# Performance work log

Hardware: AMD Instinct MI355X
Metric: run time of the kernel (lower is better)

The kernel has to match this reference:

```python
import jax, jax.numpy as jnp
import numpy as np

B = 4096      # batch
D = 256       # flattened input feature dim
NUMFEAT = 1 + D + D * (D + 1) // 2  # 33153: bias + linear + quadratic terms


def setup_inputs() -> dict:
    key = jax.random.key(0)
    k1, k2 = jax.random.split(key)
    x = jax.random.normal(k1, (B, D), dtype=jnp.float32)
    # nn.Linear(numfeat, 10, bias=False): weight shape (10, numfeat)
    W = jax.random.normal(k2, (10, NUMFEAT), dtype=jnp.float32) * 0.01
    return {"x": x, "W": W}


def reference(x, W):
    # x: (B, D) -- original does x.view(B, -1); already 2D here.
    b, d = x.shape
    # sklearn PolynomialFeatures(degree=2) column order:
    # [1, x_0..x_{d-1}, x_0*x_0, x_0*x_1, ..., x_{d-1}*x_{d-1}]
    # i.e. combinations_with_replacement == upper-triangular (incl. diagonal)
    iu0, iu1 = np.triu_indices(d)  # static index constants
    ones = jnp.ones((b, 1), dtype=x.dtype)
    cross = x[:, iu0] * x[:, iu1]          # (B, D*(D+1)/2)
    feats = jnp.concatenate([ones, x, cross], axis=1)  # (B, NUMFEAT)
    return feats @ W.T                      # (B, 10)
```

## Files before the change

### kernel.cpp

```cpp
#include <hip/hip_runtime.h>


#define DD 256
#define NF 33153
#define TPB 256
#define ASTRIDE 264

typedef __attribute__((ext_vector_type(8))) short short8;
typedef __attribute__((ext_vector_type(4))) float floatx4;
typedef __attribute__((ext_vector_type(4), aligned(4))) float float4a;

union S8U { unsigned u[4]; short8 s; };

__device__ inline unsigned pack2(float lo, float hi) {
    unsigned a = __builtin_bit_cast(unsigned, hi) + 0x8000u;
    unsigned b = __builtin_bit_cast(unsigned, lo) + 0x8000u;
    return __builtin_amdgcn_perm(a, b, 0x07060302u);
}

__global__ __launch_bounds__(TPB)
void PolynomialRegression_75385265979710_kernel(const float* __restrict__ x,
                                                const float* __restrict__ W,
                                                float* __restrict__ out) {
    __shared__ __align__(16) unsigned short As[64 * ASTRIDE];
    __shared__ float red[4 * 64];

    const int tid  = threadIdx.x;
    const int lane = tid & 63, wave = tid >> 6;
    const int ln   = lane & 15, quad = lane >> 4;
    const int q8   = quad * 8;
    const int rowbase = blockIdx.x * 64;
    const int o  = blockIdx.y;
    const int g1 = wave, g2 = 7 - wave;

#pragma unroll
    for (int it = 0; it < 8; ++it) {
        int idx = it * 2048 + tid * 8;
        int r = idx >> 8, c = idx & 255;
        const float* src = &x[(rowbase + r) * DD + c];
        float4a v0 = *(const float4a*)src;
        float4a v1 = *(const float4a*)(src + 4);
        S8U p;
        p.u[0] = pack2(v0.x, v0.y); p.u[1] = pack2(v0.z, v0.w);
        p.u[2] = pack2(v1.x, v1.y); p.u[3] = pack2(v1.z, v1.w);
        *(short8*)&As[r * ASTRIDE + c] = p.s;
    }
    __syncthreads();

    int iRow[4], bBase[4];
#pragma unroll
    for (int nt = 0; nt < 4; ++nt) {
        int g = (nt < 2) ? g1 : g2;
        int i = g * 32 + (nt & 1) * 16 + ln;
        iRow[nt]  = i;
        bBase[nt] = o * NF + 257 + i * 255 - ((i * (i - 1)) >> 1);
    }

    floatx4 acc[4][4];
#pragma unroll
    for (int mt = 0; mt < 4; ++mt)
#pragma unroll
        for (int nt = 0; nt < 4; ++nt) acc[mt][nt] = (floatx4)0.f;

    auto loadA = [&](int kk, short8* a) {
#pragma unroll
        for (int mt = 0; mt < 4; ++mt)
            a[mt] = *(const short8*)&As[(mt * 16 + ln) * ASTRIDE + kk + q8];
    };
    auto loadB = [&](int nt, int kk) -> short8 {
        const float* p = &W[bBase[nt] + kk + q8];
        float4a w0 = *(const float4a*)p;
        float4a w1 = *(const float4a*)(p + 4);
        S8U r;
        r.u[0] = pack2(w0.x, w0.y); r.u[1] = pack2(w0.z, w0.w);
        r.u[2] = pack2(w1.x, w1.y); r.u[3] = pack2(w1.z, w1.w);
        return r.s;
    };
    auto loadBmask = [&](int nt, int kk) -> short8 {
        int di = iRow[nt] - kk;
        const float* p = &W[bBase[nt] + kk + q8];
        float4a w0 = *(const float4a*)p;
        float4a w1 = *(const float4a*)(p + 4);
        float f[8] = {w0.x, w0.y, w0.z, w0.w, w1.x, w1.y, w1.z, w1.w};
#pragma unroll
        for (int e = 0; e < 8; ++e)
            if (q8 + e < di) f[e] = 0.f;
        S8U r;
        r.u[0] = pack2(f[0], f[1]); r.u[1] = pack2(f[2], f[3]);
        r.u[2] = pack2(f[4], f[5]); r.u[3] = pack2(f[6], f[7]);
        return r.s;
    };
    auto mfma2 = [&](short8* a, short8 b0, short8 b1, int nlo) {
#pragma unroll
        for (int mt = 0; mt < 4; ++mt) {
            acc[mt][nlo]     = __builtin_amdgcn_mfma_f32_16x16x32_bf16(a[mt], b0, acc[mt][nlo],     0, 0, 0);
            acc[mt][nlo + 1] = __builtin_amdgcn_mfma_f32_16x16x32_bf16(a[mt], b1, acc[mt][nlo + 1], 0, 0, 0);
        }
    };

    {
        short8 a[4];
        loadA(g1 * 32, a);
        mfma2(a, loadBmask(0, g1 * 32), loadBmask(1, g1 * 32), 0);
        loadA(g2 * 32, a);
        mfma2(a, loadBmask(2, g2 * 32), loadBmask(3, g2 * 32), 2);
    }
    for (int c = g1 + 1; c <= g2; ++c) {
        short8 a[4];
        loadA(c * 32, a);
        mfma2(a, loadB(0, c * 32), loadB(1, c * 32), 0);
    }
    for (int c = g2 + 1; c < 8; ++c) {
        short8 a[4];
        loadA(c * 32, a);
        mfma2(a, loadB(0, c * 32), loadB(1, c * 32), 0);
        mfma2(a, loadB(2, c * 32), loadB(3, c * 32), 2);
    }

    float w1v[4];
#pragma unroll
    for (int nt = 0; nt < 4; ++nt)
        w1v[nt] = W[o * NF + 1 + iRow[nt]];

#pragma unroll
    for (int mt = 0; mt < 4; ++mt) {
#pragma unroll
        for (int r = 0; r < 4; ++r) {
            const int m = mt * 16 + quad * 4 + r;
            float p = 0.f;
#pragma unroll
            for (int nt = 0; nt < 4; ++nt) {
                float xv = x[(rowbase + m) * DD + iRow[nt]];
                p = fmaf(xv, acc[mt][nt][r] + w1v[nt], p);
            }
            p += __shfl_xor(p, 1);
            p += __shfl_xor(p, 2);
            p += __shfl_xor(p, 4);
            p += __shfl_xor(p, 8);
            if (ln == 0) red[wave * 64 + m] = p;
        }
    }
    __syncthreads();

    if (tid < 64) {
        float s = red[tid] + red[64 + tid] + red[128 + tid] + red[192 + tid] + W[o * NF];
        out[(rowbase + tid) * 10 + o] = s;
    }
}

extern "C" void kernel_launch(void* const* d_in, const int* in_sizes, int n_in,
                              void* d_out, int out_size, void* d_ws, size_t ws_size,
                              hipStream_t stream) {
    const float* x = (const float*)d_in[0];
    const float* W = (const float*)d_in[1];
    float* out = (float*)d_out;

    dim3 grid(4096 / 64, 10);
    PolynomialRegression_75385265979710_kernel<<<grid, TPB, 0, stream>>>(x, W, out);
}
```

Baseline: 71.65 us.

## Prebuild masked bf16 upper-triangular weight matrix in workspace before main GEMM

A new preprocessing kernel expands the packed triangular quadratic weights into a dense, zero-masked bf16 256x256 matrix per output, stored in the workspace. The main kernel then loads B fragments directly as aligned bf16 vectors instead of doing unaligned fp32 loads with per-element masking and packing. The epilogue now reads x from the bf16 shared-memory tile instead of global memory, and launch bounds request two blocks per CU. The cost is an extra kernel launch plus writing and reading about 1.3 MB of weights, and the epilogue now uses bf16-rounded x values.

```diff
diff --git a/kernel.cpp b/kernel.cpp
--- a/kernel.cpp
+++ b/kernel.cpp
@@ -12,6 +12,10 @@
 
 union S8U { unsigned u[4]; short8 s; };
 
+__device__ inline unsigned short f2bf(float f) {
+    unsigned u = __builtin_bit_cast(unsigned, f);
+    return (unsigned short)((u + 0x7FFFu + ((u >> 16) & 1u)) >> 16);
+}
 __device__ inline unsigned pack2(float lo, float hi) {
     unsigned a = __builtin_bit_cast(unsigned, hi) + 0x8000u;
     unsigned b = __builtin_bit_cast(unsigned, lo) + 0x8000u;
@@ -19,8 +23,19 @@
 }
 
 __global__ __launch_bounds__(TPB)
+void gbuild_kernel(const float* __restrict__ W, unsigned short* __restrict__ G) {
+    int oi = blockIdx.x;
+    int o = oi >> 8, i = oi & 255;
+    int j = threadIdx.x;
+    int base = o * NF + 257 + i * DD - (i * (i - 1)) / 2 - i;
+    float v = (j >= i) ? W[base + j] : 0.f;
+    G[oi * DD + j] = f2bf(v);
+}
+
+__global__ __launch_bounds__(TPB, 2)
 void PolynomialRegression_75385265979710_kernel(const float* __restrict__ x,
                                                 const float* __restrict__ W,
+                                                const unsigned short* __restrict__ G,
                                                 float* __restrict__ out) {
     __shared__ __align__(16) unsigned short As[64 * ASTRIDE];
     __shared__ float red[4 * 64];
@@ -32,6 +47,7 @@
     const int rowbase = blockIdx.x * 64;
     const int o  = blockIdx.y;
     const int g1 = wave, g2 = 7 - wave;
+    const int rem = 8 - wave;
 
 #pragma unroll
     for (int it = 0; it < 8; ++it) {
@@ -47,80 +63,49 @@
     }
     __syncthreads();
 
-    int iRow[4], bBase[4];
-#pragma unroll
-    for (int nt = 0; nt < 4; ++nt) {
-        int g = (nt < 2) ? g1 : g2;
-        int i = g * 32 + (nt & 1) * 16 + ln;
-        iRow[nt]  = i;
-        bBase[nt] = o * NF + 257 + i * 255 - ((i * (i - 1)) >> 1);
-    }
-
     floatx4 acc[4][4];
 #pragma unroll
     for (int mt = 0; mt < 4; ++mt)
 #pragma unroll
         for (int nt = 0; nt < 4; ++nt) acc[mt][nt] = (floatx4)0.f;
 
-    auto loadA = [&](int kk, short8* a) {
+    const unsigned short* Gy = G + (o * DD) * DD;
+
+#pragma unroll
+    for (int t = 0; t < 9; ++t) {
+        const bool first = (t < rem);
+        const int g  = first ? g1 : g2;
+        const int kc = first ? (g1 + t) : (g2 + (t - rem));
+        const unsigned short* gb = Gy + (g * 32 + ln) * DD + kc * 32 + q8;
+        short8 b0 = *(const short8*)gb;
+        short8 b1 = *(const short8*)(gb + 16 * DD);
+        short8 a[4];
 #pragma unroll
         for (int mt = 0; mt < 4; ++mt)
-            a[mt] = *(const short8*)&As[(mt * 16 + ln) * ASTRIDE + kk + q8];
-    };
-    auto loadB = [&](int nt, int kk) -> short8 {
-        const float* p = &W[bBase[nt] + kk + q8];
-        float4a w0 = *(const float4a*)p;
-        float4a w1 = *(const float4a*)(p + 4);
-        S8U r;
-        r.u[0] = pack2(w0.x, w0.y); r.u[1] = pack2(w0.z, w0.w);
-        r.u[2] = pack2(w1.x, w1.y); r.u[3] = pack2(w1.z, w1.w);
-        return r.s;
-    };
-    auto loadBmask = [&](int nt, int kk) -> short8 {
-        int di = iRow[nt] - kk;
-        const float* p = &W[bBase[nt] + kk + q8];
-        float4a w0 = *(const float4a*)p;
-        float4a w1 = *(const float4a*)(p + 4);
-        float f[8] = {w0.x, w0.y, w0.z, w0.w, w1.x, w1.y, w1.z, w1.w};
+            a[mt] = *(const short8*)&As[(mt * 16 + ln) * ASTRIDE + kc * 32 + q8];
+        if (first) {
 #pragma unroll
-        for (int e = 0; e < 8; ++e)
-            if (q8 + e < di) f[e] = 0.f;
-        S8U r;
-        r.u[0] = pack2(f[0], f[1]); r.u[1] = pack2(f[2], f[3]);
-        r.u[2] = pack2(f[4], f[5]); r.u[3] = pack2(f[6], f[7]);
-        return r.s;
-    };
-    auto mfma2 = [&](short8* a, short8 b0, short8 b1, int nlo) {
+            for (int mt = 0; mt < 4; ++mt) {
+                acc[mt][0] = __builtin_amdgcn_mfma_f32_16x16x32_bf16(a[mt], b0, acc[mt][0], 0, 0, 0);
+                acc[mt][1] = __builtin_amdgcn_mfma_f32_16x16x32_bf16(a[mt], b1, acc[mt][1], 0, 0, 0);
+            }
+        } else {
 #pragma unroll
-        for (int mt = 0; mt < 4; ++mt) {
-            acc[mt][nlo]     = __builtin_amdgcn_mfma_f32_16x16x32_bf16(a[mt], b0, acc[mt][nlo],     0, 0, 0);
-            acc[mt][nlo + 1] = __builtin_amdgcn_mfma_f32_16x16x32_bf16(a[mt], b1, acc[mt][nlo + 1], 0, 0, 0);
+            for (int mt = 0; mt < 4; ++mt) {
+                acc[mt][2] = __builtin_amdgcn_mfma_f32_16x16x32_bf16(a[mt], b0, acc[mt][2], 0, 0, 0);
+                acc[mt][3] = __builtin_amdgcn_mfma_f32_16x16x32_bf16(a[mt], b1, acc[mt][3], 0, 0, 0);
+            }
         }
-    };
-
-    {
-        short8 a[4];
-        loadA(g1 * 32, a);
-        mfma2(a, loadBmask(0, g1 * 32), loadBmask(1, g1 * 32), 0);
-        loadA(g2 * 32, a);
-        mfma2(a, loadBmask(2, g2 * 32), loadBmask(3, g2 * 32), 2);
-    }
-    for (int c = g1 + 1; c <= g2; ++c) {
-        short8 a[4];
-        loadA(c * 32, a);
-        mfma2(a, loadB(0, c * 32), loadB(1, c * 32), 0);
-    }
-    for (int c = g2 + 1; c < 8; ++c) {
-        short8 a[4];
-        loadA(c * 32, a);
-        mfma2(a, loadB(0, c * 32), loadB(1, c * 32), 0);
-        mfma2(a, loadB(2, c * 32), loadB(3, c * 32), 2);
     }
 
+    int iRow[4];
     float w1v[4];
 #pragma unroll
-    for (int nt = 0; nt < 4; ++nt)
-        w1v[nt] = W[o * NF + 1 + iRow[nt]];
+    for (int nt = 0; nt < 4; ++nt) {
+        int g = (nt < 2) ? g1 : g2;
+        iRow[nt] = g * 32 + (nt & 1) * 16 + ln;
+        w1v[nt]  = W[o * NF + 1 + iRow[nt]];
+    }
 
 #pragma unroll
     for (int mt = 0; mt < 4; ++mt) {
@@ -130,7 +115,8 @@
             float p = 0.f;
 #pragma unroll
             for (int nt = 0; nt < 4; ++nt) {
-                float xv = x[(rowbase + m) * DD + iRow[nt]];
+                unsigned u = As[m * ASTRIDE + iRow[nt]];
+                float xv = __builtin_bit_cast(float, u << 16);
                 p = fmaf(xv, acc[mt][nt][r] + w1v[nt], p);
             }
             p += __shfl_xor(p, 1);
@@ -143,7 +129,8 @@
     __syncthreads();
 
     if (tid < 64) {
-        float s = red[tid] + red[64 + tid] + red[128 + tid] + red[192 + tid] + W[o * NF];
+        float s = red[tid] + red[64 + tid] + red[128 + tid] + red[192 + tid]
+                + W[o * NF];
         out[(rowbase + tid) * 10 + o] = s;
     }
 }
@@ -155,6 +142,10 @@
     const float* W = (const float*)d_in[1];
     float* out = (float*)d_out;
 
+    unsigned short* G = (unsigned short*)d_ws;
+
+    gbuild_kernel<<<10 * DD, TPB, 0, stream>>>(W, G);
+
     dim3 grid(4096 / 64, 10);
-    PolynomialRegression_75385265979710_kernel<<<grid, TPB, 0, stream>>>(x, W, out);
+    PolynomialRegression_75385265979710_kernel<<<grid, TPB, 0, stream>>>(x, W, G, out);
 }
```

Result: faster. 70.06 us (-2.2%).
